# Performance work log

Measured on AMD Instinct MI355X. Metric: run time of the kernel, lower is better.

## Reference

```python
import jax, jax.numpy as jnp
import numpy as np

B, S, E = 2, 2048, 1024
H, D = 16, 64


def setup_inputs() -> dict:
    key = jax.random.key(0)
    ks = jax.random.split(key, 9)
    s_in = 1.0 / np.sqrt(E)
    s_out = 1.0 / np.sqrt(H * D)
    return {
        "x": jax.random.normal(ks[0], (B, S, E), dtype=jnp.float32),
        "W_q": jax.random.uniform(ks[1], (H, E, D), jnp.float32, -s_in, s_in),
        "b_q": jax.random.uniform(ks[2], (H, D), jnp.float32, -s_in, s_in),
        "W_k": jax.random.uniform(ks[3], (H, E, D), jnp.float32, -s_in, s_in),
        "b_k": jax.random.uniform(ks[4], (H, D), jnp.float32, -s_in, s_in),
        "W_v": jax.random.uniform(ks[5], (H, E, D), jnp.float32, -s_in, s_in),
        "b_v": jax.random.uniform(ks[6], (H, D), jnp.float32, -s_in, s_in),
        "W_o": jax.random.uniform(ks[7], (H * D, E), jnp.float32, -s_out, s_out),
        "b_o": jax.random.uniform(ks[8], (E,), jnp.float32, -s_out, s_out),
    }


def reference(x, W_q, b_q, W_k, b_k, W_v, b_v, W_o, b_o):
    # batched per-head projections: [B,S,E] x [H,E,D] -> [B,H,S,D]
    q = jnp.einsum("bse,hed->bhsd", x, W_q) + b_q[None, :, None, :]
    k = jnp.einsum("bse,hed->bhsd", x, W_k) + b_k[None, :, None, :]
    v = jnp.einsum("bse,hed->bhsd", x, W_v) + b_v[None, :, None, :]
    scale = 1.0 / jnp.sqrt(jnp.asarray(D, dtype=x.dtype))
    score = jnp.einsum("bhsd,bhtd->bhst", q, k) * scale  # [B,H,S,S]
    causal = jnp.tril(jnp.ones((S, S), dtype=bool))
    score = jnp.where(causal[None, None], score, -jnp.inf)
    w = jax.nn.softmax(score, axis=-1)
    o = jnp.einsum("bhst,bhtd->bhsd", w, v)  # [B,H,S,D]
    # concat heads along last dim (head-major order matches torch.cat)
    o = o.transpose(0, 2, 1, 3).reshape(B, S, H * D)
    # dropout is identity in eval mode
    return o @ W_o + b_o
```

## Files before the change

### kernel.cpp

```cpp
#include <hip/hip_runtime.h>


typedef __attribute__((ext_vector_type(8)))  __bf16 bf16x8;
typedef __attribute__((ext_vector_type(4)))  __bf16 bf16x4;
typedef __attribute__((ext_vector_type(2)))  __bf16 bf16x2;
typedef __attribute__((ext_vector_type(4)))  float  f32x4;
typedef __attribute__((ext_vector_type(16))) float  f32x16;
typedef __attribute__((ext_vector_type(2)))  unsigned int u32x2;
typedef __attribute__((ext_vector_type(4)))  unsigned int u32x4;

#define LOG2E 1.4426950408889634f
#define SM_SC (0.125f * LOG2E)

static __device__ __forceinline__ void gl2lds16(const void* g, void* l) {
    __builtin_amdgcn_global_load_lds(
        (__attribute__((address_space(1))) void*)(void*)g,
        (__attribute__((address_space(3))) void*)l, 16, 0, 0);
}

static __device__ __forceinline__ unsigned pku(float a, float b) {
    bf16x2 t = { (__bf16)a, (__bf16)b };
    return __builtin_bit_cast(unsigned, t);
}

__global__ void prep_x_kern(const float* __restrict__ x, __bf16* __restrict__ xb) {
    int i = (blockIdx.x * 256 + threadIdx.x) * 4;
    f32x4 v = *(const f32x4*)(x + i);
    bf16x4 o = { (__bf16)v[0], (__bf16)v[1], (__bf16)v[2], (__bf16)v[3] };
    *(bf16x4*)(xb + i) = o;
}

__global__ void __launch_bounds__(256)
prep_w_kern(const float* __restrict__ Wq, const float* __restrict__ Wk,
            const float* __restrict__ Wv, const float* __restrict__ bq,
            const float* __restrict__ bk, const float* __restrict__ bv,
            const float* __restrict__ Wo,
            __bf16* __restrict__ wt, float* __restrict__ bias,
            __bf16* __restrict__ wto) {
    __shared__ float T[64][65];
    const int t = threadIdx.x;
    if ((int)blockIdx.x < 768) {
        const int blk = blockIdx.x;
        const int kt = blk & 15, ph = blk >> 4;
        const int h = ph & 15, p = ph >> 4;
        const float* W  = (p == 0) ? Wq : (p == 1) ? Wk : Wv;
        const float* bb = (p == 0) ? bq : (p == 1) ? bk : bv;
        #pragma unroll
        for (int i = 0; i < 4; ++i) {
            int flat = i * 1024 + t * 4;
            int kr = flat >> 6, d4 = flat & 63;
            f32x4 v = *(const f32x4*)(W + (h << 16) + ((kt * 64 + kr) << 6) + d4);
            T[kr][d4] = v[0]; T[kr][d4 + 1] = v[1]; T[kr][d4 + 2] = v[2]; T[kr][d4 + 3] = v[3];
        }
        __syncthreads();
        const int d = t >> 2, kq = (t & 3) << 4;
        bf16x8 o0, o1;
        #pragma unroll
        for (int j = 0; j < 8; ++j) o0[j] = (__bf16)T[kq + j][d];
        #pragma unroll
        for (int j = 0; j < 8; ++j) o1[j] = (__bf16)T[kq + 8 + j][d];
        __bf16* dst = wt + (((size_t)(p * 1024 + h * 64 + d)) << 10) + kt * 64 + kq;
        *(bf16x8*)dst = o0;
        *(bf16x8*)(dst + 8) = o1;
        if (kt == 0 && t < 64) bias[p * 1024 + h * 64 + t] = bb[h * 64 + t];
    } else {
        const int blk = blockIdx.x - 768;
        const int nt = blk & 15, ktile = blk >> 4;
        #pragma unroll
        for (int i = 0; i < 4; ++i) {
            int flat = i * 1024 + t * 4;
            int kr = flat >> 6, n4 = flat & 63;
            f32x4 v = *(const f32x4*)(Wo + ((size_t)(ktile * 64 + kr) << 10) + nt * 64 + n4);
            T[kr][n4] = v[0]; T[kr][n4 + 1] = v[1]; T[kr][n4 + 2] = v[2]; T[kr][n4 + 3] = v[3];
        }
        __syncthreads();
        const int n = t >> 2, kq = (t & 3) << 4;
        bf16x8 o0, o1;
        #pragma unroll
        for (int j = 0; j < 8; ++j) o0[j] = (__bf16)T[kq + j][n];
        #pragma unroll
        for (int j = 0; j < 8; ++j) o1[j] = (__bf16)T[kq + 8 + j][n];
        __bf16* dst = wto + (((size_t)(nt * 64 + n)) << 10) + ktile * 64 + kq;
        *(bf16x8*)dst = o0;
        *(bf16x8*)(dst + 8) = o1;
    }
}

template <int EPI>
__global__ void __launch_bounds__(256, 2)
gemm_bt(const __bf16* __restrict__ A, const __bf16* __restrict__ Bt,
        const float* __restrict__ bias,
        __bf16* __restrict__ outq, __bf16* __restrict__ outk, __bf16* __restrict__ outv,
        float* __restrict__ outf)
{
    __shared__ __align__(16) __bf16 As[128 * 64];
    __shared__ __align__(16) __bf16 Bs[128 * 64];
    const int tid = threadIdx.x;
    const int wid = tid >> 6, lane = tid & 63;
    const int r = lane & 15, g = lane >> 4;
    const int m0 = blockIdx.y << 7, n0 = blockIdx.x << 7;
    const int wr = wid >> 1, wc = wid & 1;
    f32x4 acc[4][4] = {};
    for (int k0 = 0; k0 < 1024; k0 += 64) {
        #pragma unroll
        for (int c = 0; c < 4; ++c) {
            int cq = (c * 4 + wid) * 64 + lane;
            int row = cq >> 3, ci = cq & 7;
            gl2lds16(A  + (((size_t)(m0 + row)) << 10) + k0 + ci * 8, As + (c * 4 + wid) * 512);
            gl2lds16(Bt + (((size_t)(n0 + row)) << 10) + k0 + ci * 8, Bs + (c * 4 + wid) * 512);
        }
        __syncthreads();
        bf16x8 af[2][4], bfr[2][4];
        #pragma unroll
        for (int kh = 0; kh < 2; ++kh)
            #pragma unroll
            for (int i = 0; i < 4; ++i) {
                af[kh][i]  = *(const bf16x8*)&As[(wr * 64 + i * 16 + r) * 64 + kh * 32 + g * 8];
                bfr[kh][i] = *(const bf16x8*)&Bs[(wc * 64 + i * 16 + r) * 64 + kh * 32 + g * 8];
            }
        #pragma unroll
        for (int kh = 0; kh < 2; ++kh)
            #pragma unroll
            for (int mi = 0; mi < 4; ++mi)
                #pragma unroll
                for (int ni = 0; ni < 4; ++ni)
                    acc[mi][ni] = __builtin_amdgcn_mfma_f32_16x16x32_bf16(
                        af[kh][mi], bfr[kh][ni], acc[mi][ni], 0, 0, 0);
        __syncthreads();
    }
    if (EPI == 0) {
        #pragma unroll
        for (int ni = 0; ni < 4; ++ni) {
            int n = n0 + wc * 64 + ni * 16 + r;
            float bv = bias[n];
            int p = n >> 10, rem = n & 1023, h = rem >> 6, d = rem & 63;
            #pragma unroll
            for (int mi = 0; mi < 4; ++mi) {
                int mb = m0 + wr * 64 + mi * 16 + g * 4;
                int b = mb >> 11, s = mb & 2047;
                f32x4 v = acc[mi][ni];
                if (p < 2) {
                    __bf16* dst = (p == 0) ? outq : outk;
                    size_t base = (((size_t)(b * 16 + h)) * 2048 + s) * 64 + d;
                    #pragma unroll
                    for (int j = 0; j < 4; ++j)
                        dst[base + (size_t)j * 64] = (__bf16)(v[j] + bv);
                } else {
                    bf16x4 pk = { (__bf16)(v[0] + bv), (__bf16)(v[1] + bv),
                                  (__bf16)(v[2] + bv), (__bf16)(v[3] + bv) };
                    *(bf16x4*)&outv[(((size_t)(b * 16 + h)) * 64 + d) * 2048 + s] = pk;
                }
            }
        }
    } else {
        #pragma unroll
        for (int ni = 0; ni < 4; ++ni) {
            int n = n0 + wc * 64 + ni * 16 + r;
            float bv = bias[n];
            #pragma unroll
            for (int mi = 0; mi < 4; ++mi) {
                int mb = m0 + wr * 64 + mi * 16 + g * 4;
                f32x4 v = acc[mi][ni];
                #pragma unroll
                for (int j = 0; j < 4; ++j)
                    outf[((size_t)(mb + j) << 10) + n] = v[j] + bv;
            }
        }
    }
}

__global__ void __launch_bounds__(256, 3)
attn_kern(const __bf16* __restrict__ q, const __bf16* __restrict__ k,
          const __bf16* __restrict__ vT, __bf16* __restrict__ pO0,
          __bf16* __restrict__ pO1, float* __restrict__ ml)
{
    __shared__ __align__(16) __bf16 Ks [2][64][72];
    __shared__ __align__(16) __bf16 VsT[2][64][72];
    const int tid = threadIdx.x, lane = tid & 63, w = tid >> 6;
    const int r31 = lane & 31, hi = lane >> 5;
    const int x = blockIdx.x & 7, kvh = blockIdx.x >> 3;
    const int bh = blockIdx.y, b = bh >> 4, h = bh & 15;
    const __bf16* qh  = q  + ((size_t)bh << 17);
    const __bf16* khp = k  + ((size_t)bh << 17);
    const __bf16* vhp = vT + ((size_t)bh << 17);
    __bf16* pO = kvh ? pO1 : pO0;
    const int srow = tid >> 3, sci = tid & 7;

    for (int seg = 0; seg < 2; ++seg) {
        const int xq = (seg == 0) ? (15 - x) : x;
        const int qb0 = xq << 7;
        const int wrow0 = qb0 + w * 32;
        const int mg = wrow0 + r31;
        const int tbeg = kvh * (xq + 1), tend = tbeg + (xq + 1);

        bf16x8 qf[4];
        #pragma unroll
        for (int kk = 0; kk < 4; ++kk)
            qf[kk] = *(const bf16x8*)&qh[(size_t)mg * 64 + kk * 16 + hi * 8];

        f32x16 oacc[2] = {};
        f32x16 lacc = {};
        float mrun = -3.0e38f;
        bf16x8 onesf;
        #pragma unroll
        for (int j = 0; j < 8; ++j) onesf[j] = (__bf16)1.0f;

        #pragma unroll
        for (int it = 0; it < 2; ++it) {
            int row = srow + it * 32;
            *(bf16x8*)&Ks [0][row][sci * 8] = *(const bf16x8*)&khp[(size_t)(tbeg * 64 + row) * 64 + sci * 8];
            *(bf16x8*)&VsT[0][row][sci * 8] = *(const bf16x8*)&vhp[(size_t)row * 2048 + tbeg * 64 + sci * 8];
        }
        __syncthreads();

        for (int t = tbeg; t < tend; ++t) {
            const int cur = (t - tbeg) & 1, nxt = cur ^ 1;
            const int n0 = t << 6;
            const bool pre = (t + 1 < tend);
            bf16x8 nk[2], nv[2];
            if (pre) {
                int n1 = n0 + 64;
                #pragma unroll
                for (int it = 0; it < 2; ++it) {
                    int row = srow + it * 32;
                    nk[it] = *(const bf16x8*)&khp[(size_t)(n1 + row) * 64 + sci * 8];
                    nv[it] = *(const bf16x8*)&vhp[(size_t)row * 2048 + n1 + sci * 8];
                }
            }
            if (n0 <= wrow0 + 31) {
                f32x16 sacc[2] = {};
                __builtin_amdgcn_s_setprio(1);
                #pragma unroll
                for (int kk = 0; kk < 4; ++kk) {
                    bf16x8 kf0 = *(const bf16x8*)&Ks[cur][r31]     [kk * 16 + hi * 8];
                    bf16x8 kf1 = *(const bf16x8*)&Ks[cur][32 + r31][kk * 16 + hi * 8];
                    sacc[0] = __builtin_amdgcn_mfma_f32_32x32x16_bf16(kf0, qf[kk], sacc[0], 0, 0, 0);
                    sacc[1] = __builtin_amdgcn_mfma_f32_32x32x16_bf16(kf1, qf[kk], sacc[1], 0, 0, 0);
                }
                __builtin_amdgcn_s_setprio(0);
                if (n0 + 63 > wrow0) {
                    #pragma unroll
                    for (int nf = 0; nf < 2; ++nf)
                        #pragma unroll
                        for (int i = 0; i < 16; ++i) {
                            int n = n0 + nf * 32 + (i & 3) + 8 * (i >> 2) + 4 * hi;
                            if (n > mg) sacc[nf][i] = -3.0e38f;
                        }
                }
                float mx[16];
                #pragma unroll
                for (int i = 0; i < 16; ++i) mx[i] = fmaxf(sacc[0][i], sacc[1][i]);
                #pragma unroll
                for (int s = 8; s > 0; s >>= 1)
                    #pragma unroll
                    for (int i = 0; i < 8; ++i)
                        if (i < s) mx[i] = fmaxf(mx[i], mx[i + s]);
                float pmh = mx[0];
                if (!__all((pmh - mrun) * SM_SC <= 8.0f)) {
                    float pm = fmaxf(pmh, __shfl_xor(pmh, 32));
                    float mnew = fmaxf(mrun, pm);
                    float fac = exp2f((mrun - mnew) * SM_SC);
                    lacc[0] *= fac;
                    #pragma unroll
                    for (int df = 0; df < 2; ++df)
                        #pragma unroll
                        for (int i = 0; i < 16; ++i) oacc[df][i] *= fac;
                    mrun = mnew;
                }
                #pragma unroll
                for (int nf = 0; nf < 2; ++nf)
                    #pragma unroll
                    for (int i = 0; i < 16; ++i)
                        sacc[nf][i] = exp2f((sacc[nf][i] - mrun) * SM_SC);
                #pragma unroll
                for (int nf = 0; nf < 2; ++nf) {
                    unsigned pk[8];
                    #pragma unroll
                    for (int j = 0; j < 8; ++j)
                        pk[j] = pku(sacc[nf][2 * j], sacc[nf][2 * j + 1]);
#if __has_builtin(__builtin_amdgcn_permlane32_swap)
                    u32x2 s02 = __builtin_amdgcn_permlane32_swap(pk[0], pk[2], false, false);
                    u32x2 s13 = __builtin_amdgcn_permlane32_swap(pk[1], pk[3], false, false);
                    u32x2 s46 = __builtin_amdgcn_permlane32_swap(pk[4], pk[6], false, false);
                    u32x2 s57 = __builtin_amdgcn_permlane32_swap(pk[5], pk[7], false, false);
                    u32x4 fw0 = { s02[0], s13[0], s02[1], s13[1] };
                    u32x4 fw1 = { s46[0], s57[0], s46[1], s57[1] };
#else
                    unsigned rxa = __shfl_xor(hi ? pk[0] : pk[2], 32);
                    unsigned rxb = __shfl_xor(hi ? pk[1] : pk[3], 32);
                    unsigned rxc = __shfl_xor(hi ? pk[4] : pk[6], 32);
                    unsigned rxd = __shfl_xor(hi ? pk[5] : pk[7], 32);
                    u32x4 fw0 = { hi ? rxa : pk[0], hi ? rxb : pk[1],
                                  hi ? pk[2] : rxa, hi ? pk[3] : rxb };
                    u32x4 fw1 = { hi ? rxc : pk[4], hi ? rxd : pk[5],
                                  hi ? pk[6] : rxc, hi ? pk[7] : rxd };
#endif
                    bf16x8 pf0 = __builtin_bit_cast(bf16x8, fw0);
                    bf16x8 pf1 = __builtin_bit_cast(bf16x8, fw1);
                    __builtin_amdgcn_s_setprio(1);
                    #pragma unroll
                    for (int kl = 0; kl < 2; ++kl) {
                        const bf16x8 pf = kl ? pf1 : pf0;
                        const int kk = nf * 2 + kl;
                        bf16x8 af0 = *(const bf16x8*)&VsT[cur][r31]     [kk * 16 + hi * 8];
                        bf16x8 af1 = *(const bf16x8*)&VsT[cur][32 + r31][kk * 16 + hi * 8];
                        oacc[0] = __builtin_amdgcn_mfma_f32_32x32x16_bf16(af0, pf, oacc[0], 0, 0, 0);
                        oacc[1] = __builtin_amdgcn_mfma_f32_32x32x16_bf16(af1, pf, oacc[1], 0, 0, 0);
                        lacc    = __builtin_amdgcn_mfma_f32_32x32x16_bf16(onesf, pf, lacc, 0, 0, 0);
                    }
                    __builtin_amdgcn_s_setprio(0);
                }
            }
            if (pre) {
                #pragma unroll
                for (int it = 0; it < 2; ++it) {
                    int row = srow + it * 32;
                    *(bf16x8*)&Ks [nxt][row][sci * 8] = nk[it];
                    *(bf16x8*)&VsT[nxt][row][sci * 8] = nv[it];
                }
            }
            __syncthreads();
        }
        float lrun = lacc[0];
        float inv = (lrun > 0.f) ? 1.0f / lrun : 0.f;
        #pragma unroll
        for (int df = 0; df < 2; ++df)
            #pragma unroll
            for (int td = 0; td < 8; ++td) {
                bf16x2 pr = { (__bf16)(oacc[df][2 * td] * inv),
                              (__bf16)(oacc[df][2 * td + 1] * inv) };
                int d = df * 32 + 8 * (td >> 1) + 4 * hi + 2 * (td & 1);
                *(bf16x2*)&pO[((size_t)(b * 2048 + mg) << 10) + h * 64 + d] = pr;
            }
        if (hi == 0) {
            size_t mi = (((size_t)kvh * 32 + bh) * 2048 + mg) * 2;
            ml[mi] = mrun;
            ml[mi + 1] = lrun;
        }
    }
}

__global__ void merge_kern(const __bf16* __restrict__ pO0, const float* __restrict__ ml,
                           __bf16* __restrict__ ob)
{
    int i = blockIdx.x * 256 + threadIdx.x;
    int m = i >> 7, rem = i & 127, h = rem >> 3, d8 = (rem & 7) * 8;
    int bh = (m >> 11) * 16 + h, sr = m & 2047;
    size_t i0 = ((size_t)bh * 2048 + sr) * 2;
    float m0 = ml[i0], l0 = ml[i0 + 1];
    float m1 = ml[131072 + i0], l1 = ml[131072 + i0 + 1];
    float mx = fmaxf(m0, m1);
    float c0 = exp2f((m0 - mx) * SM_SC) * l0;
    float c1 = exp2f((m1 - mx) * SM_SC) * l1;
    float inv = 1.0f / (c0 + c1);
    float w0 = c0 * inv, w1 = c1 * inv;
    size_t off = (size_t)m * 1024 + h * 64 + d8;
    bf16x8 a = *(const bf16x8*)(pO0 + off);
    bf16x8 c = *(const bf16x8*)(ob + off);
    bf16x8 r;
    #pragma unroll
    for (int j = 0; j < 8; ++j) r[j] = (__bf16)(w0 * (float)a[j] + w1 * (float)c[j]);
    *(bf16x8*)(ob + off) = r;
}

extern "C" void kernel_launch(void* const* d_in, const int* in_sizes, int n_in,
                              void* d_out, int out_size, void* d_ws, size_t ws_size,
                              hipStream_t stream) {
    const float* x  = (const float*)d_in[0];
    const float* Wq = (const float*)d_in[1];
    const float* bq = (const float*)d_in[2];
    const float* Wk = (const float*)d_in[3];
    const float* bk = (const float*)d_in[4];
    const float* Wv = (const float*)d_in[5];
    const float* bv = (const float*)d_in[6];
    const float* Wo = (const float*)d_in[7];
    const float* bo = (const float*)d_in[8];
    float* out = (float*)d_out;
    char* ws = (char*)d_ws;
    __bf16* xb    = (__bf16*)(ws + 0);
    __bf16* wtqkv = (__bf16*)(ws + 8388608);
    __bf16* wot   = (__bf16*)(ws + 14680064);
    float*  biasq = (float*) (ws + 16777216);
    __bf16* qb    = (__bf16*)(ws + 16793600);
    __bf16* kb    = (__bf16*)(ws + 25182208);
    __bf16* vtb   = (__bf16*)(ws + 33570816);
    __bf16* ob    = (__bf16*)(ws + 41959424);
    __bf16* pO0   = xb;
    float*  mlbuf = (float*)(ws + 8388608);

    prep_x_kern<<<4096, 256, 0, stream>>>(x, xb);
    prep_w_kern<<<1024, 256, 0, stream>>>(Wq, Wk, Wv, bq, bk, bv, Wo, wtqkv, biasq, wot);
    gemm_bt<0><<<dim3(24, 32), 256, 0, stream>>>(xb, wtqkv, biasq, qb, kb, vtb, nullptr);
    attn_kern<<<dim3(16, 32), 256, 0, stream>>>(qb, kb, vtb, pO0, ob, mlbuf);
    merge_kern<<<4096, 256, 0, stream>>>(pO0, mlbuf, ob);
    gemm_bt<1><<<dim3(8, 32), 256, 0, stream>>>(ob, wot, bo, nullptr, nullptr, nullptr, out);
}
```

Measured before the change: 130.5 us.

## Merge prep kernels and split attention into one q-tile per block

Folds the x conversion and weight transposes into a single prep launch, which removes one kernel launch. The attention kernel no longer pairs q-tiles (15-x, x) inside one block. It launches twice as many blocks, each handling one q-tile and one kv half, ordered heaviest first. The s_setprio hints around the MFMA loops are also removed. The added parallelism comes at the cost of unbalanced per-block work, which relies on the hardware scheduler to even out.

```diff
diff --git a/kernel.cpp b/kernel.cpp
--- a/kernel.cpp
+++ b/kernel.cpp
@@ -23,24 +23,23 @@
     return __builtin_bit_cast(unsigned, t);
 }
 
-__global__ void prep_x_kern(const float* __restrict__ x, __bf16* __restrict__ xb) {
-    int i = (blockIdx.x * 256 + threadIdx.x) * 4;
-    f32x4 v = *(const f32x4*)(x + i);
-    bf16x4 o = { (__bf16)v[0], (__bf16)v[1], (__bf16)v[2], (__bf16)v[3] };
-    *(bf16x4*)(xb + i) = o;
-}
-
 __global__ void __launch_bounds__(256)
-prep_w_kern(const float* __restrict__ Wq, const float* __restrict__ Wk,
-            const float* __restrict__ Wv, const float* __restrict__ bq,
-            const float* __restrict__ bk, const float* __restrict__ bv,
-            const float* __restrict__ Wo,
-            __bf16* __restrict__ wt, float* __restrict__ bias,
-            __bf16* __restrict__ wto) {
+prep_all_kern(const float* __restrict__ x, const float* __restrict__ Wq,
+              const float* __restrict__ Wk, const float* __restrict__ Wv,
+              const float* __restrict__ bq, const float* __restrict__ bk,
+              const float* __restrict__ bv, const float* __restrict__ Wo,
+              __bf16* __restrict__ xb, __bf16* __restrict__ wt,
+              float* __restrict__ bias, __bf16* __restrict__ wto) {
     __shared__ float T[64][65];
     const int t = threadIdx.x;
-    if ((int)blockIdx.x < 768) {
-        const int blk = blockIdx.x;
+    const int bx = blockIdx.x;
+    if (bx < 4096) {
+        int i = (bx * 256 + t) * 4;
+        f32x4 v = *(const f32x4*)(x + i);
+        bf16x4 o = { (__bf16)v[0], (__bf16)v[1], (__bf16)v[2], (__bf16)v[3] };
+        *(bf16x4*)(xb + i) = o;
+    } else if (bx < 4864) {
+        const int blk = bx - 4096;
         const int kt = blk & 15, ph = blk >> 4;
         const int h = ph & 15, p = ph >> 4;
         const float* W  = (p == 0) ? Wq : (p == 1) ? Wk : Wv;
@@ -64,7 +63,7 @@
         *(bf16x8*)(dst + 8) = o1;
         if (kt == 0 && t < 64) bias[p * 1024 + h * 64 + t] = bb[h * 64 + t];
     } else {
-        const int blk = blockIdx.x - 768;
+        const int blk = bx - 4864;
         const int nt = blk & 15, ktile = blk >> 4;
         #pragma unroll
         for (int i = 0; i < 4; ++i) {
@@ -178,7 +177,8 @@
     __shared__ __align__(16) __bf16 VsT[2][64][72];
     const int tid = threadIdx.x, lane = tid & 63, w = tid >> 6;
     const int r31 = lane & 31, hi = lane >> 5;
-    const int x = blockIdx.x & 7, kvh = blockIdx.x >> 3;
+    const int bx = blockIdx.x;
+    const int j = 15 - (bx >> 1), kvh = bx & 1;
     const int bh = blockIdx.y, b = bh >> 4, h = bh & 15;
     const __bf16* qh  = q  + ((size_t)bh << 17);
     const __bf16* khp = k  + ((size_t)bh << 17);
@@ -186,157 +186,150 @@
     __bf16* pO = kvh ? pO1 : pO0;
     const int srow = tid >> 3, sci = tid & 7;
 
-    for (int seg = 0; seg < 2; ++seg) {
-        const int xq = (seg == 0) ? (15 - x) : x;
-        const int qb0 = xq << 7;
-        const int wrow0 = qb0 + w * 32;
-        const int mg = wrow0 + r31;
-        const int tbeg = kvh * (xq + 1), tend = tbeg + (xq + 1);
-
-        bf16x8 qf[4];
-        #pragma unroll
-        for (int kk = 0; kk < 4; ++kk)
-            qf[kk] = *(const bf16x8*)&qh[(size_t)mg * 64 + kk * 16 + hi * 8];
-
-        f32x16 oacc[2] = {};
-        f32x16 lacc = {};
-        float mrun = -3.0e38f;
-        bf16x8 onesf;
-        #pragma unroll
-        for (int j = 0; j < 8; ++j) onesf[j] = (__bf16)1.0f;
-
-        #pragma unroll
-        for (int it = 0; it < 2; ++it) {
-            int row = srow + it * 32;
-            *(bf16x8*)&Ks [0][row][sci * 8] = *(const bf16x8*)&khp[(size_t)(tbeg * 64 + row) * 64 + sci * 8];
-            *(bf16x8*)&VsT[0][row][sci * 8] = *(const bf16x8*)&vhp[(size_t)row * 2048 + tbeg * 64 + sci * 8];
-        }
-        __syncthreads();
-
-        for (int t = tbeg; t < tend; ++t) {
-            const int cur = (t - tbeg) & 1, nxt = cur ^ 1;
-            const int n0 = t << 6;
-            const bool pre = (t + 1 < tend);
-            bf16x8 nk[2], nv[2];
-            if (pre) {
-                int n1 = n0 + 64;
-                #pragma unroll
-                for (int it = 0; it < 2; ++it) {
-                    int row = srow + it * 32;
-                    nk[it] = *(const bf16x8*)&khp[(size_t)(n1 + row) * 64 + sci * 8];
-                    nv[it] = *(const bf16x8*)&vhp[(size_t)row * 2048 + n1 + sci * 8];
-                }
-            }
-            if (n0 <= wrow0 + 31) {
-                f32x16 sacc[2] = {};
-                __builtin_amdgcn_s_setprio(1);
-                #pragma unroll
-                for (int kk = 0; kk < 4; ++kk) {
-                    bf16x8 kf0 = *(const bf16x8*)&Ks[cur][r31]     [kk * 16 + hi * 8];
-                    bf16x8 kf1 = *(const bf16x8*)&Ks[cur][32 + r31][kk * 16 + hi * 8];
-                    sacc[0] = __builtin_amdgcn_mfma_f32_32x32x16_bf16(kf0, qf[kk], sacc[0], 0, 0, 0);
-                    sacc[1] = __builtin_amdgcn_mfma_f32_32x32x16_bf16(kf1, qf[kk], sacc[1], 0, 0, 0);
-                }
-                __builtin_amdgcn_s_setprio(0);
-                if (n0 + 63 > wrow0) {
-                    #pragma unroll
-                    for (int nf = 0; nf < 2; ++nf)
-                        #pragma unroll
-                        for (int i = 0; i < 16; ++i) {
-                            int n = n0 + nf * 32 + (i & 3) + 8 * (i >> 2) + 4 * hi;
-                            if (n > mg) sacc[nf][i] = -3.0e38f;
-                        }
-                }
-                float mx[16];
-                #pragma unroll
-                for (int i = 0; i < 16; ++i) mx[i] = fmaxf(sacc[0][i], sacc[1][i]);
-                #pragma unroll
-                for (int s = 8; s > 0; s >>= 1)
-                    #pragma unroll
-                    for (int i = 0; i < 8; ++i)
-                        if (i < s) mx[i] = fmaxf(mx[i], mx[i + s]);
-                float pmh = mx[0];
-                if (!__all((pmh - mrun) * SM_SC <= 8.0f)) {
-                    float pm = fmaxf(pmh, __shfl_xor(pmh, 32));
-                    float mnew = fmaxf(mrun, pm);
-                    float fac = exp2f((mrun - mnew) * SM_SC);
-                    lacc[0] *= fac;
-                    #pragma unroll
-                    for (int df = 0; df < 2; ++df)
-                        #pragma unroll
-                        for (int i = 0; i < 16; ++i) oacc[df][i] *= fac;
-                    mrun = mnew;
-                }
+    const int qb0 = j << 7;
+    const int wrow0 = qb0 + w * 32;
+    const int mg = wrow0 + r31;
+    const int tbeg = kvh * (j + 1), tend = tbeg + (j + 1);
+
+    bf16x8 qf[4];
+    #pragma unroll
+    for (int kk = 0; kk < 4; ++kk)
+        qf[kk] = *(const bf16x8*)&qh[(size_t)mg * 64 + kk * 16 + hi * 8];
+
+    f32x16 oacc[2] = {};
+    f32x16 lacc = {};
+    float mrun = -3.0e38f;
+    bf16x8 onesf;
+    #pragma unroll
+    for (int jj = 0; jj < 8; ++jj) onesf[jj] = (__bf16)1.0f;
+
+    #pragma unroll
+    for (int it = 0; it < 2; ++it) {
+        int row = srow + it * 32;
+        *(bf16x8*)&Ks [0][row][sci * 8] = *(const bf16x8*)&khp[(size_t)(tbeg * 64 + row) * 64 + sci * 8];
+        *(bf16x8*)&VsT[0][row][sci * 8] = *(const bf16x8*)&vhp[(size_t)row * 2048 + tbeg * 64 + sci * 8];
+    }
+    __syncthreads();
+
+    for (int t = tbeg; t < tend; ++t) {
+        const int cur = (t - tbeg) & 1, nxt = cur ^ 1;
+        const int n0 = t << 6;
+        const bool pre = (t + 1 < tend);
+        bf16x8 nk[2], nv[2];
+        if (pre) {
+            int n1 = n0 + 64;
+            #pragma unroll
+            for (int it = 0; it < 2; ++it) {
+                int row = srow + it * 32;
+                nk[it] = *(const bf16x8*)&khp[(size_t)(n1 + row) * 64 + sci * 8];
+                nv[it] = *(const bf16x8*)&vhp[(size_t)row * 2048 + n1 + sci * 8];
+            }
+        }
+        if (n0 <= wrow0 + 31) {
+            f32x16 sacc[2] = {};
+            #pragma unroll
+            for (int kk = 0; kk < 4; ++kk) {
+                bf16x8 kf0 = *(const bf16x8*)&Ks[cur][r31]     [kk * 16 + hi * 8];
+                bf16x8 kf1 = *(const bf16x8*)&Ks[cur][32 + r31][kk * 16 + hi * 8];
+                sacc[0] = __builtin_amdgcn_mfma_f32_32x32x16_bf16(kf0, qf[kk], sacc[0], 0, 0, 0);
+                sacc[1] = __builtin_amdgcn_mfma_f32_32x32x16_bf16(kf1, qf[kk], sacc[1], 0, 0, 0);
+            }
+            if (n0 + 63 > wrow0) {
                 #pragma unroll
                 for (int nf = 0; nf < 2; ++nf)
                     #pragma unroll
-                    for (int i = 0; i < 16; ++i)
-                        sacc[nf][i] = exp2f((sacc[nf][i] - mrun) * SM_SC);
-                #pragma unroll
-                for (int nf = 0; nf < 2; ++nf) {
-                    unsigned pk[8];
+                    for (int i = 0; i < 16; ++i) {
+                        int n = n0 + nf * 32 + (i & 3) + 8 * (i >> 2) + 4 * hi;
+                        if (n > mg) sacc[nf][i] = -3.0e38f;
+                    }
+            }
+            float mx[16];
+            #pragma unroll
+            for (int i = 0; i < 16; ++i) mx[i] = fmaxf(sacc[0][i], sacc[1][i]);
+            #pragma unroll
+            for (int s = 8; s > 0; s >>= 1)
+                #pragma unroll
+                for (int i = 0; i < 8; ++i)
+                    if (i < s) mx[i] = fmaxf(mx[i], mx[i + s]);
+            float pmh = mx[0];
+            if (!__all((pmh - mrun) * SM_SC <= 8.0f)) {
+                float pm = fmaxf(pmh, __shfl_xor(pmh, 32));
+                float mnew = fmaxf(mrun, pm);
+                float fac = exp2f((mrun - mnew) * SM_SC);
+                lacc[0] *= fac;
+                #pragma unroll
+                for (int df = 0; df < 2; ++df)
                     #pragma unroll
-                    for (int j = 0; j < 8; ++j)
-                        pk[j] = pku(sacc[nf][2 * j], sacc[nf][2 * j + 1]);
+                    for (int i = 0; i < 16; ++i) oacc[df][i] *= fac;
+                mrun = mnew;
+            }
+            #pragma unroll
+            for (int nf = 0; nf < 2; ++nf)
+                #pragma unroll
+                for (int i = 0; i < 16; ++i)
+                    sacc[nf][i] = exp2f((sacc[nf][i] - mrun) * SM_SC);
+            #pragma unroll
+            for (int nf = 0; nf < 2; ++nf) {
+                unsigned pk[8];
+                #pragma unroll
+                for (int jj = 0; jj < 8; ++jj)
+                    pk[jj] = pku(sacc[nf][2 * jj], sacc[nf][2 * jj + 1]);
 #if __has_builtin(__builtin_amdgcn_permlane32_swap)
-                    u32x2 s02 = __builtin_amdgcn_permlane32_swap(pk[0], pk[2], false, false);
-                    u32x2 s13 = __builtin_amdgcn_permlane32_swap(pk[1], pk[3], false, false);
-                    u32x2 s46 = __builtin_amdgcn_permlane32_swap(pk[4], pk[6], false, false);
-                    u32x2 s57 = __builtin_amdgcn_permlane32_swap(pk[5], pk[7], false, false);
-                    u32x4 fw0 = { s02[0], s13[0], s02[1], s13[1] };
-                    u32x4 fw1 = { s46[0], s57[0], s46[1], s57[1] };
+                u32x2 s02 = __builtin_amdgcn_permlane32_swap(pk[0], pk[2], false, false);
+                u32x2 s13 = __builtin_amdgcn_permlane32_swap(pk[1], pk[3], false, false);
+                u32x2 s46 = __builtin_amdgcn_permlane32_swap(pk[4], pk[6], false, false);
+                u32x2 s57 = __builtin_amdgcn_permlane32_swap(pk[5], pk[7], false, false);
+                u32x4 fw0 = { s02[0], s13[0], s02[1], s13[1] };
+                u32x4 fw1 = { s46[0], s57[0], s46[1], s57[1] };
 #else
-                    unsigned rxa = __shfl_xor(hi ? pk[0] : pk[2], 32);
-                    unsigned rxb = __shfl_xor(hi ? pk[1] : pk[3], 32);
-                    unsigned rxc = __shfl_xor(hi ? pk[4] : pk[6], 32);
-                    unsigned rxd = __shfl_xor(hi ? pk[5] : pk[7], 32);
-                    u32x4 fw0 = { hi ? rxa : pk[0], hi ? rxb : pk[1],
-                                  hi ? pk[2] : rxa, hi ? pk[3] : rxb };
-                    u32x4 fw1 = { hi ? rxc : pk[4], hi ? rxd : pk[5],
-                                  hi ? pk[6] : rxc, hi ? pk[7] : rxd };
+                unsigned rxa = __shfl_xor(hi ? pk[0] : pk[2], 32);
+                unsigned rxb = __shfl_xor(hi ? pk[1] : pk[3], 32);
+                unsigned rxc = __shfl_xor(hi ? pk[4] : pk[6], 32);
+                unsigned rxd = __shfl_xor(hi ? pk[5] : pk[7], 32);
+                u32x4 fw0 = { hi ? rxa : pk[0], hi ? rxb : pk[1],
+                              hi ? pk[2] : rxa, hi ? pk[3] : rxb };
+                u32x4 fw1 = { hi ? rxc : pk[4], hi ? rxd : pk[5],
+                              hi ? pk[6] : rxc, hi ? pk[7] : rxd };
 #endif
-                    bf16x8 pf0 = __builtin_bit_cast(bf16x8, fw0);
-                    bf16x8 pf1 = __builtin_bit_cast(bf16x8, fw1);
-                    __builtin_amdgcn_s_setprio(1);
-                    #pragma unroll
-                    for (int kl = 0; kl < 2; ++kl) {
-                        const bf16x8 pf = kl ? pf1 : pf0;
-                        const int kk = nf * 2 + kl;
-                        bf16x8 af0 = *(const bf16x8*)&VsT[cur][r31]     [kk * 16 + hi * 8];
-                        bf16x8 af1 = *(const bf16x8*)&VsT[cur][32 + r31][kk * 16 + hi * 8];
-                        oacc[0] = __builtin_amdgcn_mfma_f32_32x32x16_bf16(af0, pf, oacc[0], 0, 0, 0);
-                        oacc[1] = __builtin_amdgcn_mfma_f32_32x32x16_bf16(af1, pf, oacc[1], 0, 0, 0);
-                        lacc    = __builtin_amdgcn_mfma_f32_32x32x16_bf16(onesf, pf, lacc, 0, 0, 0);
-                    }
-                    __builtin_amdgcn_s_setprio(0);
+                bf16x8 pf0 = __builtin_bit_cast(bf16x8, fw0);
+                bf16x8 pf1 = __builtin_bit_cast(bf16x8, fw1);
+                #pragma unroll
+                for (int kl = 0; kl < 2; ++kl) {
+                    const bf16x8 pf = kl ? pf1 : pf0;
+                    const int kk = nf * 2 + kl;
+                    bf16x8 af0 = *(const bf16x8*)&VsT[cur][r31]     [kk * 16 + hi * 8];
+                    bf16x8 af1 = *(const bf16x8*)&VsT[cur][32 + r31][kk * 16 + hi * 8];
+                    oacc[0] = __builtin_amdgcn_mfma_f32_32x32x16_bf16(af0, pf, oacc[0], 0, 0, 0);
+                    oacc[1] = __builtin_amdgcn_mfma_f32_32x32x16_bf16(af1, pf, oacc[1], 0, 0, 0);
+                    lacc    = __builtin_amdgcn_mfma_f32_32x32x16_bf16(onesf, pf, lacc, 0, 0, 0);
                 }
             }
-            if (pre) {
-                #pragma unroll
-                for (int it = 0; it < 2; ++it) {
-                    int row = srow + it * 32;
-                    *(bf16x8*)&Ks [nxt][row][sci * 8] = nk[it];
-                    *(bf16x8*)&VsT[nxt][row][sci * 8] = nv[it];
-                }
-            }
-            __syncthreads();
-        }
-        float lrun = lacc[0];
-        float inv = (lrun > 0.f) ? 1.0f / lrun : 0.f;
-        #pragma unroll
-        for (int df = 0; df < 2; ++df)
-            #pragma unroll
-            for (int td = 0; td < 8; ++td) {
-                bf16x2 pr = { (__bf16)(oacc[df][2 * td] * inv),
-                              (__bf16)(oacc[df][2 * td + 1] * inv) };
-                int d = df * 32 + 8 * (td >> 1) + 4 * hi + 2 * (td & 1);
-                *(bf16x2*)&pO[((size_t)(b * 2048 + mg) << 10) + h * 64 + d] = pr;
-            }
-        if (hi == 0) {
-            size_t mi = (((size_t)kvh * 32 + bh) * 2048 + mg) * 2;
-            ml[mi] = mrun;
-            ml[mi + 1] = lrun;
-        }
+        }
+        if (pre) {
+            #pragma unroll
+            for (int it = 0; it < 2; ++it) {
+                int row = srow + it * 32;
+                *(bf16x8*)&Ks [nxt][row][sci * 8] = nk[it];
+                *(bf16x8*)&VsT[nxt][row][sci * 8] = nv[it];
+            }
+        }
+        __syncthreads();
+    }
+    float lrun = lacc[0];
+    float inv = (lrun > 0.f) ? 1.0f / lrun : 0.f;
+    #pragma unroll
+    for (int df = 0; df < 2; ++df)
+        #pragma unroll
+        for (int td = 0; td < 8; ++td) {
+            bf16x2 pr = { (__bf16)(oacc[df][2 * td] * inv),
+                          (__bf16)(oacc[df][2 * td + 1] * inv) };
+            int d = df * 32 + 8 * (td >> 1) + 4 * hi + 2 * (td & 1);
+            *(bf16x2*)&pO[((size_t)(b * 2048 + mg) << 10) + h * 64 + d] = pr;
+        }
+    if (hi == 0) {
+        size_t mi = (((size_t)kvh * 32 + bh) * 2048 + mg) * 2;
+        ml[mi] = mrun;
+        ml[mi + 1] = lrun;
     }
 }
 
@@ -388,10 +381,10 @@
     __bf16* pO0   = xb;
     float*  mlbuf = (float*)(ws + 8388608);
 
-    prep_x_kern<<<4096, 256, 0, stream>>>(x, xb);
-    prep_w_kern<<<1024, 256, 0, stream>>>(Wq, Wk, Wv, bq, bk, bv, Wo, wtqkv, biasq, wot);
+    prep_all_kern<<<5120, 256, 0, stream>>>(x, Wq, Wk, Wv, bq, bk, bv, Wo,
+                                            xb, wtqkv, biasq, wot);
     gemm_bt<0><<<dim3(24, 32), 256, 0, stream>>>(xb, wtqkv, biasq, qb, kb, vtb, nullptr);
-    attn_kern<<<dim3(16, 32), 256, 0, stream>>>(qb, kb, vtb, pO0, ob, mlbuf);
+    attn_kern<<<dim3(32, 32), 256, 0, stream>>>(qb, kb, vtb, pO0, ob, mlbuf);
     merge_kern<<<4096, 256, 0, stream>>>(pO0, mlbuf, ob);
     gemm_bt<1><<<dim3(8, 32), 256, 0, stream>>>(ob, wot, bo, nullptr, nullptr, nullptr, out);
 }
```

Measured after the change: 150.5 us. +15.3%, slower.
